# Performance work log

Hardware: AMD Instinct MI355X
Metric: run time of the kernel (lower is better)

Reference implementation:

```python
import jax, jax.numpy as jnp
import numpy as np

N, E, FS = 50000, 400000, 256
H, D = 8, 64            # GAT heads, hidden_size (per-head out_feats)
NH, DK, DV = 8, 64, 64  # transformer MHA
B = 1024
NEG_SLOPE = 0.2
EPS = 1e-6


def _layer_norm(x, g, b, eps=EPS):
    mu = x.mean(-1, keepdims=True)
    var = x.var(-1, keepdims=True)
    return (x - mu) / jnp.sqrt(var + eps) * g + b


def setup_inputs() -> dict:
    key = jax.random.key(0)
    ks = jax.random.split(key, 20)
    s = 0.02
    return {
        "features": jax.random.normal(ks[0], (N, FS), jnp.float32),
        "src": jax.random.randint(ks[1], (E,), 0, N, jnp.int32),
        "dst": jax.random.randint(ks[2], (E,), 0, N, jnp.int32),
        "url": jax.random.randint(ks[3], (B,), 1, N + 1, jnp.int32),  # 1-based ids
        # GATConv params (DGL-style)
        "gat_fc_w": jax.random.normal(ks[4], (FS, H * D), jnp.float32) * s,
        "attn_l": jax.random.normal(ks[5], (H, D), jnp.float32) * s,
        "attn_r": jax.random.normal(ks[6], (H, D), jnp.float32) * s,
        "gat_res_w": jax.random.normal(ks[7], (FS, H * D), jnp.float32) * s,
        "gat_bias": jnp.zeros((H, D), jnp.float32),
        # post-GAT LayerNorm
        "ln_g": jnp.ones((D,), jnp.float32),
        "ln_b": jnp.zeros((D,), jnp.float32),
        # MultiHeadAttention params
        "wq": jax.random.normal(ks[8], (D, NH * DK), jnp.float32) * s,
        "wk": jax.random.normal(ks[9], (D, NH * DK), jnp.float32) * s,
        "wv": jax.random.normal(ks[10], (D, NH * DV), jnp.float32) * s,
        "fc_w": jax.random.normal(ks[11], (NH * DV, D), jnp.float32) * s,
        "fc_b": jnp.zeros((D,), jnp.float32),
        "mha_ln_g": jnp.ones((D,), jnp.float32),
        "mha_ln_b": jnp.zeros((D,), jnp.float32),
        # final classifier
        "out_w": jax.random.normal(ks[12], (D, 2), jnp.float32) * s,
        "out_b": jnp.zeros((2,), jnp.float32),
    }


def reference(features, src, dst, url, gat_fc_w, attn_l, attn_r, gat_res_w,
              gat_bias, ln_g, ln_b, wq, wk, wv, fc_w, fc_b, mha_ln_g,
              mha_ln_b, out_w, out_b):
    # ---- GATConv (residual=True, bias, negative_slope=0.2, no activation) ----
    feat = (features @ gat_fc_w).reshape(N, H, D)          # [N,H,D]
    el = jnp.einsum('nhd,hd->nh', feat, attn_l)            # [N,H]
    er = jnp.einsum('nhd,hd->nh', feat, attn_r)            # [N,H]
    e = jax.nn.leaky_relu(el[src] + er[dst], NEG_SLOPE)    # [E,H] edge scores
    # segment softmax over incoming edges of each dst node
    m = jax.ops.segment_max(e, dst, num_segments=N)        # [N,H]
    m = jnp.where(jnp.isfinite(m), m, 0.0)
    ex = jnp.exp(e - m[dst])                               # [E,H]
    denom = jax.ops.segment_sum(ex, dst, num_segments=N)   # [N,H]
    a = ex / jnp.maximum(denom[dst], 1e-20)                # [E,H]
    msg = feat[src] * a[:, :, None]                        # [E,H,D]
    rst = jax.ops.segment_sum(msg, dst, num_segments=N)    # [N,H,D]
    res = (features @ gat_res_w).reshape(N, H, D)
    gat_emb = rst + res + gat_bias                         # [N,H,D]

    # ---- select batch nodes (url is 1-based) ----
    ids = url - 1
    x = gat_emb[ids]                                       # [B,H,D]
    x = _layer_norm(x, ln_g, ln_b)

    # ---- dense multi-head self-attention over the H gat heads (seq dim) ----
    residual = x
    q = (x @ wq).reshape(B, H, NH, DK)
    k = (x @ wk).reshape(B, H, NH, DK)
    v = (x @ wv).reshape(B, H, NH, DV)
    attn = jnp.einsum('bqhd,bkhd->bhqk', q, k) / jnp.sqrt(jnp.float32(DK))
    attn = jax.nn.softmax(attn, axis=-1)
    o = jnp.einsum('bhqk,bkhd->bqhd', attn, v).reshape(B, H, NH * DV)
    o = o @ fc_w + fc_b                                    # [B,H,D]
    o = _layer_norm(o + residual, mha_ln_g, mha_ln_b)

    # ---- pool + classify ----
    pooled = o.sum(axis=1)                                 # [B,D]
    logits = pooled @ out_w + out_b                        # [B,2]
    return logits
```

## Files before the change

kernel.cpp:

```cpp
#include <hip/hip_runtime.h>
#include <math.h>

#define Nn 50000
#define Ee 400000
#define FSz 256
#define HD_ 512
#define Bb 1024
#define HSZ 2048

static __device__ __forceinline__ int clampi(int v, int lo, int hi){
    return v < lo ? lo : (v > hi ? hi : v);
}
static __device__ __forceinline__ unsigned short f2bf(float f){
    unsigned int u = __float_as_uint(f);
    unsigned int r = u + 0x7FFFu + ((u >> 16) & 1u);
    return (unsigned short)(r >> 16);
}
static __device__ __forceinline__ float bflo(unsigned int v){ return __uint_as_float(v << 16); }
static __device__ __forceinline__ float bfhi(unsigned int v){ return __uint_as_float(v & 0xFFFF0000u); }

__global__ __launch_bounds__(256) void k_scatter(const int* __restrict__ src, const int* __restrict__ dst,
                                                 const int* __restrict__ url,
                                                 int* __restrict__ fill, int* __restrict__ slist,
                                                 const float* __restrict__ W,
                                                 const float* __restrict__ al,
                                                 const float* __restrict__ ar,
                                                 float* __restrict__ wl, float* __restrict__ wr,
                                                 const float* __restrict__ Wfc,
                                                 const float* __restrict__ Wres,
                                                 unsigned int* __restrict__ wfcb,
                                                 unsigned int* __restrict__ wresb){
    int t = threadIdx.x;
    if(blockIdx.x >= 1579){
        int bi = blockIdx.x - 1579;
        int m = bi >> 4;
        const float2* Sf = (const float2*)(m ? Wres : Wfc);
        unsigned int* D = m ? wresb : wfcb;
        int base = (bi & 15) * 8192;
        #pragma unroll
        for(int i = 0; i < 32; i++){
            int idx = base + i*256 + t;
            float2 v = Sf[idx];
            D[idx] = ((unsigned int)f2bf(v.y) << 16) | (unsigned int)f2bf(v.x);
        }
        return;
    }
    if(blockIdx.x >= 1563){
        int bi = blockIdx.x - 1563;
        int wv = t >> 6, lane = t & 63;
        #pragma unroll
        for(int r = 0; r < 4; r++){
            int f = bi*16 + wv*4 + r;
            float pl[8], pr[8];
            #pragma unroll
            for(int h = 0; h < 8; h++){
                float w = W[f*512 + h*64 + lane];
                pl[h] = w * al[h*64 + lane];
                pr[h] = w * ar[h*64 + lane];
            }
            #pragma unroll
            for(int h = 0; h < 8; h++){
                #pragma unroll
                for(int m = 32; m >= 1; m >>= 1){
                    pl[h] += __shfl_xor(pl[h], m, 64);
                    pr[h] += __shfl_xor(pr[h], m, 64);
                }
            }
            #pragma unroll
            for(int h = 0; h < 8; h++){
                if(lane == h){ wl[h*256 + f] = pl[h]; wr[h*256 + f] = pr[h]; }
            }
        }
        return;
    }
    __shared__ int key[HSZ];
    __shared__ int chainhead[HSZ];
    __shared__ short nxt[Bb];
    for(int i = t; i < HSZ; i += 256){ key[i] = -1; chainhead[i] = -1; }
    __syncthreads();
    for(int b = t; b < Bb; b += 256){
        int n = clampi(url[b] - 1, 0, Nn - 1);
        int h = n & (HSZ - 1);
        while(true){
            int prev = atomicCAS(&key[h], -1, n);
            if(prev == -1 || prev == n) break;
            h = (h + 1) & (HSZ - 1);
        }
        int old = atomicExch(&chainhead[h], b);
        nxt[b] = (short)old;
    }
    __syncthreads();
    int e = blockIdx.x * 256 + t;
    if(e >= Ee) return;
    int d = dst[e];
    if((unsigned)d >= (unsigned)Nn) return;
    int h = d & (HSZ - 1);
    while(true){
        int k = key[h];
        if(k == -1) return;
        if(k == d) break;
        h = (h + 1) & (HSZ - 1);
    }
    int s = clampi(src[e], 0, Nn - 1);
    for(int b = chainhead[h]; b != -1; b = nxt[b]){
        int pos = atomicAdd(&fill[b], 1);
        if(pos < 64) slist[b*64 + pos] = s;
    }
}

__global__ __launch_bounds__(256) void k_gat(const float* __restrict__ features,
                                             const unsigned int* __restrict__ Wfcb,
                                             const unsigned int* __restrict__ Wresb,
                                             const float* __restrict__ bias,
                                             const float* __restrict__ wl,
                                             const float* __restrict__ wr,
                                             const int* __restrict__ url,
                                             const int* __restrict__ fill, const int* __restrict__ slist,
                                             float* __restrict__ gemb){
    int t = threadIdx.x;
    int lane = t & 63, wv = t >> 6;
    int u0 = blockIdx.x * 2;

    __shared__ float cxs[2][8][256];
    __shared__ float fres[2][256];
    __shared__ float sew[2][64][8];
    __shared__ float ser[2][8];
    __shared__ int   sslist[2][64];

    for(int i = t; i < 2*64*8; i += 256) ((float*)sew)[i] = 0.f;

    float4 rwl[8], rwr[8];
    #pragma unroll
    for(int h = 0; h < 8; h++){
        rwl[h] = *(const float4*)&wl[h*256 + 4*lane];
        rwr[h] = *(const float4*)&wr[h*256 + 4*lane];
    }

    int dg[2], nj[2];
    #pragma unroll
    for(int j = 0; j < 2; j++){
        int u = u0 + j;
        dg[j] = min(fill[u], 64);
        nj[j] = clampi(url[u] - 1, 0, Nn - 1);
        if(t < dg[j]) sslist[j][t] = slist[u*64 + t];
        fres[j][t] = features[(size_t)nj[j] * FSz + t];
    }
    __syncthreads();

    int c1 = dg[0];
    int total = c1 + dg[1];
    for(int tau = wv; tau < total + 2; tau += 4){
        int j, i, isEr = 0;
        if(tau < c1){ j = 0; i = tau; }
        else if(tau < total){ j = 1; i = tau - c1; }
        else { j = tau - total; i = 0; isEr = 1; }
        int s = isEr ? nj[j] : sslist[j][i];
        float4 x = *(const float4*)(features + (size_t)s * FSz + 4*lane);
        float p[8];
        if(isEr){
            #pragma unroll
            for(int h = 0; h < 8; h++)
                p[h] = x.x*rwr[h].x + x.y*rwr[h].y + x.z*rwr[h].z + x.w*rwr[h].w;
        } else {
            #pragma unroll
            for(int h = 0; h < 8; h++)
                p[h] = x.x*rwl[h].x + x.y*rwl[h].y + x.z*rwl[h].z + x.w*rwl[h].w;
        }
        #pragma unroll
        for(int h = 0; h < 8; h++){
            #pragma unroll
            for(int m = 32; m >= 1; m >>= 1) p[h] += __shfl_xor(p[h], m, 64);
        }
        if(lane == 0){
            if(isEr){
                #pragma unroll
                for(int h = 0; h < 8; h++) ser[j][h] = p[h];
            } else {
                #pragma unroll
                for(int h = 0; h < 8; h++) sew[j][i][h] = p[h];
            }
        }
    }
    __syncthreads();
    if(t < 16){
        int j = t >> 3, h = t & 7;
        int dgj = dg[j];
        if(dgj > 0){
            float ern = ser[j][h];
            float m = -1e30f;
            for(int i = 0; i < dgj; i++){
                float v = sew[j][i][h] + ern;
                v = v > 0.f ? v : 0.2f * v;
                m = fmaxf(m, v);
            }
            float sum = 0.f;
            for(int i = 0; i < dgj; i++){
                float v = sew[j][i][h] + ern;
                v = v > 0.f ? v : 0.2f * v;
                float w = expf(v - m);
                sum += w;
                sew[j][i][h] = w;
            }
            float inv = 1.0f / fmaxf(sum, 1e-20f);
            for(int i = 0; i < dgj; i++) sew[j][i][h] *= inv;
        }
    }
    __syncthreads();
    {
        float cx[2][8];
        #pragma unroll
        for(int j = 0; j < 2; j++)
            #pragma unroll
            for(int h = 0; h < 8; h++) cx[j][h] = 0.f;
        int mxd = max(dg[0], dg[1]);
        for(int i = 0; i < mxd; i += 2){
            float x[2][2];
            #pragma unroll
            for(int j = 0; j < 2; j++)
                #pragma unroll
                for(int ii = 0; ii < 2; ii++){
                    int idx = i + ii;
                    int s = (idx < dg[j]) ? sslist[j][idx] : 0;
                    x[j][ii] = features[(size_t)s * FSz + t];
                }
            #pragma unroll
            for(int j = 0; j < 2; j++)
                #pragma unroll
                for(int ii = 0; ii < 2; ii++){
                    int idx = i + ii;
                    const float* av = &sew[j][idx < 64 ? idx : 0][0];
                    float xm = (idx < dg[j]) ? x[j][ii] : 0.f;
                    #pragma unroll
                    for(int h = 0; h < 8; h++) cx[j][h] += av[h] * xm;
                }
        }
        #pragma unroll
        for(int j = 0; j < 2; j++)
            #pragma unroll
            for(int h = 0; h < 8; h++) cxs[j][h][t] = cx[j][h];
    }
    __syncthreads();

    int h = t >> 5;
    int o0 = 2 * t;
    float a[2][2] = {{0,0},{0,0}};
    for(int f = 0; f < 256; f += 4){
        unsigned int w0 = Wfcb[(f+0)*256 + t];
        unsigned int w1 = Wfcb[(f+1)*256 + t];
        unsigned int w2 = Wfcb[(f+2)*256 + t];
        unsigned int w3 = Wfcb[(f+3)*256 + t];
        unsigned int r0 = Wresb[(f+0)*256 + t];
        unsigned int r1 = Wresb[(f+1)*256 + t];
        unsigned int r2 = Wresb[(f+2)*256 + t];
        unsigned int r3 = Wresb[(f+3)*256 + t];
        #pragma unroll
        for(int j = 0; j < 2; j++){
            float4 c = *(const float4*)&cxs[j][h][f];
            float4 x = *(const float4*)&fres[j][f];
            a[j][0] += c.x*bflo(w0) + c.y*bflo(w1) + c.z*bflo(w2) + c.w*bflo(w3)
                     + x.x*bflo(r0) + x.y*bflo(r1) + x.z*bflo(r2) + x.w*bflo(r3);
            a[j][1] += c.x*bfhi(w0) + c.y*bfhi(w1) + c.z*bfhi(w2) + c.w*bfhi(w3)
                     + x.x*bfhi(r0) + x.y*bfhi(r1) + x.z*bfhi(r2) + x.w*bfhi(r3);
        }
    }
    float b0 = bias[o0], b1 = bias[o0 + 1];
    #pragma unroll
    for(int j = 0; j < 2; j++){
        float2* gp = (float2*)(gemb + (size_t)(u0 + j) * HD_);
        gp[t] = make_float2(a[j][0] + b0, a[j][1] + b1);
    }
}

__global__ __launch_bounds__(256, 4) void k_mha(const float* __restrict__ gemb,
                                             const float* __restrict__ lng, const float* __restrict__ lnb,
                                             const float* __restrict__ wq, const float* __restrict__ wk,
                                             const float* __restrict__ wvp, const float* __restrict__ fcw,
                                             const float* __restrict__ fcb, const float* __restrict__ mlg,
                                             const float* __restrict__ mlb, const float* __restrict__ outw,
                                             const float* __restrict__ outb, float* __restrict__ out){
    __shared__ float A[512];
    __shared__ float xnF[512];
    __shared__ unsigned short xnT[512];
    __shared__ unsigned short qkb[8320];
    __shared__ float mu8[8], rs8[8], pooled[64];

    int t = threadIdx.x;
    int wv = t >> 6;
    int e = blockIdx.x;

    {
        const float* g0 = gemb + (size_t)e * HD_;
        A[t] = g0[t]; A[t + 256] = g0[t + 256];
    }
    __syncthreads();
    if(t < 64){
        int q = t >> 3, d0 = t & 7;
        float s = 0.f, s2 = 0.f;
        #pragma unroll
        for(int k = 0; k < 8; k++){ float v = A[q*64 + d0 + 8*k]; s += v; s2 += v * v; }
        #pragma unroll
        for(int m = 1; m <= 4; m <<= 1){ s += __shfl_xor(s, m, 64); s2 += __shfl_xor(s2, m, 64); }
        if(d0 == 0){
            float mu = s * (1.0f/64.0f);
            float var = s2 * (1.0f/64.0f) - mu * mu;
            mu8[q] = mu; rs8[q] = rsqrtf(fmaxf(var, 0.0f) + 1e-6f);
        }
    }
    __syncthreads();
    #pragma unroll
    for(int p = 0; p < 2; p++){
        int i = p*256 + t; int q = i >> 6, d = i & 63;
        float xv = (A[i] - mu8[q]) * rs8[q] * lng[d] + lnb[d];
        xnF[i] = xv;
        xnT[d*8 + q] = f2bf(xv);
    }
    __syncthreads();
    float aq0[8], aq1[8], ak0[8], ak1[8], av0[8], av1[8];
    #pragma unroll
    for(int r = 0; r < 8; r++){
        aq0[r]=0.f; aq1[r]=0.f; ak0[r]=0.f;
        ak1[r]=0.f; av0[r]=0.f; av1[r]=0.f;
    }
    #pragma unroll 2
    for(int d = 0; d < 64; d++){
        float q0 = wq[d*512 + t],  q1 = wq[d*512 + t + 256];
        float k0 = wk[d*512 + t],  k1 = wk[d*512 + t + 256];
        float v0 = wvp[d*512 + t], v1 = wvp[d*512 + t + 256];
        uint4 xp = *(const uint4*)&xnT[d*8];
        float xv[8] = { bflo(xp.x), bfhi(xp.x), bflo(xp.y), bfhi(xp.y),
                        bflo(xp.z), bfhi(xp.z), bflo(xp.w), bfhi(xp.w) };
        #pragma unroll
        for(int r = 0; r < 8; r++){
            aq0[r] += xv[r]*q0; aq1[r] += xv[r]*q1;
            ak0[r] += xv[r]*k0; ak1[r] += xv[r]*k1;
            av0[r] += xv[r]*v0; av1[r] += xv[r]*v1;
        }
    }
    #pragma unroll
    for(int qq = 0; qq < 8; qq++){
        qkb[qq*520 + t]              = f2bf(aq0[qq]);
        qkb[qq*520 + t + 256]        = f2bf(aq1[qq]);
        qkb[4160 + qq*520 + t]       = f2bf(ak0[qq]);
        qkb[4160 + qq*520 + t + 256] = f2bf(ak1[qq]);
    }
    __syncthreads();
    #pragma unroll
    for(int p = 0; p < 2; p++){
        int idx = p*256 + t;
        int nh = idx >> 6, qq = (idx >> 3) & 7, kk = idx & 7;
        const unsigned short* qrow = &qkb[qq*520 + nh*64];
        const unsigned short* krow = &qkb[4160 + kk*520 + nh*64];
        float s = 0.f;
        #pragma unroll
        for(int d8 = 0; d8 < 64; d8 += 8){
            uint4 qv = *(const uint4*)&qrow[d8];
            uint4 kv = *(const uint4*)&krow[d8];
            s += bflo(qv.x)*bflo(kv.x) + bfhi(qv.x)*bfhi(kv.x)
               + bflo(qv.y)*bflo(kv.y) + bfhi(qv.y)*bfhi(kv.y)
               + bflo(qv.z)*bflo(kv.z) + bfhi(qv.z)*bfhi(kv.z)
               + bflo(qv.w)*bflo(kv.w) + bfhi(qv.w)*bfhi(kv.w);
        }
        A[idx] = s * 0.125f;
    }
    __syncthreads();
    if(t < 64){
        int row = t;
        float mx = -1e30f;
        #pragma unroll
        for(int k = 0; k < 8; k++) mx = fmaxf(mx, A[row*8 + k]);
        float ev[8]; float s = 0.f;
        #pragma unroll
        for(int k = 0; k < 8; k++){ ev[k] = expf(A[row*8 + k] - mx); s += ev[k]; }
        float inv = 1.0f / s;
        #pragma unroll
        for(int k = 0; k < 8; k++) A[row*8 + k] = ev[k] * inv;
    }
    __syncthreads();
    {
        int nh0 = wv;
        #pragma unroll
        for(int qq = 0; qq < 8; qq++){
            const float* s0 = &A[nh0*64 + qq*8];
            const float* s1 = &A[(nh0+4)*64 + qq*8];
            float4 a0 = *(const float4*)s0, b0 = *(const float4*)(s0 + 4);
            float4 a1 = *(const float4*)s1, b1 = *(const float4*)(s1 + 4);
            float o0 = a0.x*av0[0] + a0.y*av0[1] + a0.z*av0[2] + a0.w*av0[3]
                     + b0.x*av0[4] + b0.y*av0[5] + b0.z*av0[6] + b0.w*av0[7];
            float o1 = a1.x*av1[0] + a1.y*av1[1] + a1.z*av1[2] + a1.w*av1[3]
                     + b1.x*av1[4] + b1.y*av1[5] + b1.z*av1[6] + b1.w*av1[7];
            qkb[qq*520 + t]       = f2bf(o0);
            qkb[qq*520 + t + 256] = f2bf(o1);
        }
    }
    __syncthreads();
    {
        float* P = (float*)&qkb[4160];
        int g = (t & 63) & 31;
        int qh = (t & 63) >> 5;
        int k0r = wv * 128;
        float a[4][2];
        #pragma unroll
        for(int jq = 0; jq < 4; jq++){ a[jq][0] = 0.f; a[jq][1] = 0.f; }
        const float2* fw2 = (const float2*)fcw;
        for(int k = k0r; k < k0r + 128; k += 8){
            float2 f0 = fw2[(k+0)*32 + g];
            float2 f1 = fw2[(k+1)*32 + g];
            float2 f2 = fw2[(k+2)*32 + g];
            float2 f3 = fw2[(k+3)*32 + g];
            float2 f4 = fw2[(k+4)*32 + g];
            float2 f5 = fw2[(k+5)*32 + g];
            float2 f6 = fw2[(k+6)*32 + g];
            float2 f7 = fw2[(k+7)*32 + g];
            #pragma unroll
            for(int jq = 0; jq < 4; jq++){
                int qq = qh*4 + jq;
                uint4 op = *(const uint4*)&qkb[qq*520 + k];
                float x0 = bflo(op.x), x1 = bfhi(op.x), x2 = bflo(op.y), x3 = bfhi(op.y);
                float x4 = bflo(op.z), x5 = bfhi(op.z), x6 = bflo(op.w), x7 = bfhi(op.w);
                a[jq][0] += x0*f0.x + x1*f1.x + x2*f2.x + x3*f3.x + x4*f4.x + x5*f5.x + x6*f6.x + x7*f7.x;
                a[jq][1] += x0*f0.y + x1*f1.y + x2*f2.y + x3*f3.y + x4*f4.y + x5*f5.y + x6*f6.y + x7*f7.y;
            }
        }
        __syncthreads();
        #pragma unroll
        for(int jq = 0; jq < 4; jq++){
            int qq = qh*4 + jq;
            *(float2*)&P[wv*512 + qq*64 + 2*g] = make_float2(a[jq][0], a[jq][1]);
        }
        __syncthreads();
        #pragma unroll
        for(int p = 0; p < 2; p++){
            int o = p*256 + t; int dd = o & 63;
            A[o] = P[o] + P[512 + o] + P[1024 + o] + P[1536 + o] + fcb[dd] + xnF[o];
        }
    }
    __syncthreads();
    if(t < 64){
        int q = t >> 3, d0 = t & 7;
        float s = 0.f, s2 = 0.f;
        #pragma unroll
        for(int k = 0; k < 8; k++){ float v = A[q*64 + d0 + 8*k]; s += v; s2 += v * v; }
        #pragma unroll
        for(int m = 1; m <= 4; m <<= 1){ s += __shfl_xor(s, m, 64); s2 += __shfl_xor(s2, m, 64); }
        if(d0 == 0){
            float mu = s * (1.0f/64.0f);
            float var = s2 * (1.0f/64.0f) - mu * mu;
            mu8[q] = mu; rs8[q] = rsqrtf(fmaxf(var, 0.0f) + 1e-6f);
        }
    }
    __syncthreads();
    if(t < 64){
        int dd = t;
        float g2 = mlg[dd], bb = mlb[dd];
        float s = 0.f;
        #pragma unroll
        for(int qq = 0; qq < 8; qq++)
            s += (A[qq*64 + dd] - mu8[qq]) * rs8[qq] * g2 + bb;
        pooled[dd] = s;
    }
    __syncthreads();
    if(t < 128){
        int c = t >> 6, d = t & 63;
        float v = pooled[d] * outw[d*2 + c];
        #pragma unroll
        for(int m = 32; m >= 1; m >>= 1) v += __shfl_xor(v, m, 64);
        if((t & 63) == 0) out[e*2 + c] = v + outb[c];
    }
}

extern "C" void kernel_launch(void* const* d_in, const int* in_sizes, int n_in,
                              void* d_out, int out_size, void* d_ws, size_t ws_size,
                              hipStream_t stream){
    (void)in_sizes; (void)n_in; (void)out_size; (void)ws_size;
    const float* features  = (const float*)d_in[0];
    const int*   src       = (const int*)d_in[1];
    const int*   dst       = (const int*)d_in[2];
    const int*   url       = (const int*)d_in[3];
    const float* gat_fc_w  = (const float*)d_in[4];
    const float* attn_l    = (const float*)d_in[5];
    const float* attn_r    = (const float*)d_in[6];
    const float* gat_res_w = (const float*)d_in[7];
    const float* gat_bias  = (const float*)d_in[8];
    const float* ln_g      = (const float*)d_in[9];
    const float* ln_b      = (const float*)d_in[10];
    const float* wq        = (const float*)d_in[11];
    const float* wk        = (const float*)d_in[12];
    const float* wv        = (const float*)d_in[13];
    const float* fc_w      = (const float*)d_in[14];
    const float* fc_b      = (const float*)d_in[15];
    const float* mha_ln_g  = (const float*)d_in[16];
    const float* mha_ln_b  = (const float*)d_in[17];
    const float* out_w     = (const float*)d_in[18];
    const float* out_b     = (const float*)d_in[19];

    char* base = (char*)d_ws;
    size_t cur = 0;
    auto alloc = [&](size_t nbytes) -> void* {
        void* p = base + cur;
        cur = (cur + nbytes + 255) & ~(size_t)255;
        return p;
    };
    float*        wl    = (float*)alloc(2048 * sizeof(float));
    float*        wr    = (float*)alloc(2048 * sizeof(float));
    int*          fill  = (int*)alloc(1024 * sizeof(int));
    int*          slist = (int*)alloc((size_t)1024 * 64 * sizeof(int));
    float*        gemb  = (float*)alloc((size_t)1024 * 512 * sizeof(float));
    unsigned int* wfcb  = (unsigned int*)alloc((size_t)256 * 512 * sizeof(unsigned short));
    unsigned int* wresb = (unsigned int*)alloc((size_t)256 * 512 * sizeof(unsigned short));

    hipMemsetAsync(fill, 0, 1024 * sizeof(int), stream);

    hipLaunchKernelGGL(k_scatter, dim3(1611), dim3(256), 0, stream, src, dst, url, fill, slist,
                       gat_fc_w, attn_l, attn_r, wl, wr, gat_fc_w, gat_res_w, wfcb, wresb);
    hipLaunchKernelGGL(k_gat,     dim3(512),  dim3(256), 0, stream, features, wfcb, wresb, gat_bias,
                       wl, wr, url, fill, slist, gemb);
    hipLaunchKernelGGL(k_mha,     dim3(1024), dim3(256), 0, stream, gemb, ln_g, ln_b,
                       wq, wk, wv, fc_w, fc_b, mha_ln_g, mha_ln_b, out_w, out_b,
                       (float*)d_out);
}
```

Baseline: 208.0 us.

## Process one batch node per GAT block and parallelize edge softmax across lanes

The GAT kernel now handles one batch node per block instead of two, doubling the grid to 1024 blocks and adding a launch bound of 4 blocks per SM. The per-head edge softmax moves from 16 serial threads to 64 threads that split edges and combine results with shuffle reductions. The aggregation loop is unrolled by 4 gathers instead of 2 per node. These changes aim to raise parallelism and occupancy and cut the serial softmax latency. In exchange, the bf16 weight matrices are streamed once per node instead of once per pair of nodes, doubling weight traffic.

```diff
diff --git a/kernel.cpp b/kernel.cpp
--- a/kernel.cpp
+++ b/kernel.cpp
@@ -108,7 +108,7 @@
     }
 }
 
-__global__ __launch_bounds__(256) void k_gat(const float* __restrict__ features,
+__global__ __launch_bounds__(256, 4) void k_gat(const float* __restrict__ features,
                                              const unsigned int* __restrict__ Wfcb,
                                              const unsigned int* __restrict__ Wresb,
                                              const float* __restrict__ bias,
@@ -119,15 +119,15 @@
                                              float* __restrict__ gemb){
     int t = threadIdx.x;
     int lane = t & 63, wv = t >> 6;
-    int u0 = blockIdx.x * 2;
-
-    __shared__ float cxs[2][8][256];
-    __shared__ float fres[2][256];
-    __shared__ float sew[2][64][8];
-    __shared__ float ser[2][8];
-    __shared__ int   sslist[2][64];
-
-    for(int i = t; i < 2*64*8; i += 256) ((float*)sew)[i] = 0.f;
+    int u = blockIdx.x;
+
+    __shared__ float cxs[8][256];
+    __shared__ float fres[256];
+    __shared__ float sew[64][8];
+    __shared__ float ser[8];
+    __shared__ int   sslist[64];
+
+    for(int i = t; i < 64*8; i += 256) ((float*)sew)[i] = 0.f;
 
     float4 rwl[8], rwr[8];
     #pragma unroll
@@ -136,25 +136,15 @@
         rwr[h] = *(const float4*)&wr[h*256 + 4*lane];
     }
 
-    int dg[2], nj[2];
-    #pragma unroll
-    for(int j = 0; j < 2; j++){
-        int u = u0 + j;
-        dg[j] = min(fill[u], 64);
-        nj[j] = clampi(url[u] - 1, 0, Nn - 1);
-        if(t < dg[j]) sslist[j][t] = slist[u*64 + t];
-        fres[j][t] = features[(size_t)nj[j] * FSz + t];
-    }
-    __syncthreads();
-
-    int c1 = dg[0];
-    int total = c1 + dg[1];
-    for(int tau = wv; tau < total + 2; tau += 4){
-        int j, i, isEr = 0;
-        if(tau < c1){ j = 0; i = tau; }
-        else if(tau < total){ j = 1; i = tau - c1; }
-        else { j = tau - total; i = 0; isEr = 1; }
-        int s = isEr ? nj[j] : sslist[j][i];
+    int dg = min(fill[u], 64);
+    int nj = clampi(url[u] - 1, 0, Nn - 1);
+    if(t < dg) sslist[t] = slist[u*64 + t];
+    fres[t] = features[(size_t)nj * FSz + t];
+    __syncthreads();
+
+    for(int tau = wv; tau < dg + 1; tau += 4){
+        int isEr = (tau == dg);
+        int s = isEr ? nj : sslist[tau];
         float4 x = *(const float4*)(features + (size_t)s * FSz + 4*lane);
         float p[8];
         if(isEr){
@@ -174,76 +164,67 @@
         if(lane == 0){
             if(isEr){
                 #pragma unroll
-                for(int h = 0; h < 8; h++) ser[j][h] = p[h];
+                for(int h = 0; h < 8; h++) ser[h] = p[h];
             } else {
                 #pragma unroll
-                for(int h = 0; h < 8; h++) sew[j][i][h] = p[h];
-            }
-        }
-    }
-    __syncthreads();
-    if(t < 16){
-        int j = t >> 3, h = t & 7;
-        int dgj = dg[j];
-        if(dgj > 0){
-            float ern = ser[j][h];
-            float m = -1e30f;
-            for(int i = 0; i < dgj; i++){
-                float v = sew[j][i][h] + ern;
-                v = v > 0.f ? v : 0.2f * v;
-                m = fmaxf(m, v);
-            }
-            float sum = 0.f;
-            for(int i = 0; i < dgj; i++){
-                float v = sew[j][i][h] + ern;
-                v = v > 0.f ? v : 0.2f * v;
-                float w = expf(v - m);
-                sum += w;
-                sew[j][i][h] = w;
-            }
-            float inv = 1.0f / fmaxf(sum, 1e-20f);
-            for(int i = 0; i < dgj; i++) sew[j][i][h] *= inv;
-        }
+                for(int h = 0; h < 8; h++) sew[tau][h] = p[h];
+            }
+        }
+    }
+    __syncthreads();
+    if(t < 64){
+        int h = t >> 3, il = t & 7;
+        float ern = ser[h];
+        float m = -1e30f;
+        for(int i = il; i < dg; i += 8){
+            float v = sew[i][h] + ern;
+            v = v > 0.f ? v : 0.2f * v;
+            m = fmaxf(m, v);
+        }
+        #pragma unroll
+        for(int mm = 1; mm <= 4; mm <<= 1) m = fmaxf(m, __shfl_xor(m, mm, 64));
+        float sum = 0.f;
+        for(int i = il; i < dg; i += 8){
+            float v = sew[i][h] + ern;
+            v = v > 0.f ? v : 0.2f * v;
+            float w = expf(v - m);
+            sum += w;
+            sew[i][h] = w;
+        }
+        #pragma unroll
+        for(int mm = 1; mm <= 4; mm <<= 1) sum += __shfl_xor(sum, mm, 64);
+        float inv = 1.0f / fmaxf(sum, 1e-20f);
+        for(int i = il; i < dg; i += 8) sew[i][h] *= inv;
     }
     __syncthreads();
     {
-        float cx[2][8];
-        #pragma unroll
-        for(int j = 0; j < 2; j++)
-            #pragma unroll
-            for(int h = 0; h < 8; h++) cx[j][h] = 0.f;
-        int mxd = max(dg[0], dg[1]);
-        for(int i = 0; i < mxd; i += 2){
-            float x[2][2];
-            #pragma unroll
-            for(int j = 0; j < 2; j++)
+        float cx[8];
+        #pragma unroll
+        for(int h = 0; h < 8; h++) cx[h] = 0.f;
+        for(int i = 0; i < dg; i += 4){
+            float x[4];
+            #pragma unroll
+            for(int ii = 0; ii < 4; ii++){
+                int idx = i + ii;
+                int s = (idx < dg) ? sslist[idx] : 0;
+                x[ii] = features[(size_t)s * FSz + t];
+            }
+            #pragma unroll
+            for(int ii = 0; ii < 4; ii++){
+                int idx = i + ii;
+                const float* av = &sew[idx < 64 ? idx : 0][0];
+                float xm = (idx < dg) ? x[ii] : 0.f;
                 #pragma unroll
-                for(int ii = 0; ii < 2; ii++){
-                    int idx = i + ii;
-                    int s = (idx < dg[j]) ? sslist[j][idx] : 0;
-                    x[j][ii] = features[(size_t)s * FSz + t];
-                }
-            #pragma unroll
-            for(int j = 0; j < 2; j++)
-                #pragma unroll
-                for(int ii = 0; ii < 2; ii++){
-                    int idx = i + ii;
-                    const float* av = &sew[j][idx < 64 ? idx : 0][0];
-                    float xm = (idx < dg[j]) ? x[j][ii] : 0.f;
-                    #pragma unroll
-                    for(int h = 0; h < 8; h++) cx[j][h] += av[h] * xm;
-                }
-        }
-        #pragma unroll
-        for(int j = 0; j < 2; j++)
-            #pragma unroll
-            for(int h = 0; h < 8; h++) cxs[j][h][t] = cx[j][h];
-    }
-    __syncthreads();
-
-    int h = t >> 5;
-    int o0 = 2 * t;
-    float a[2][2] = {{0,0},{0,0}};
+                for(int h = 0; h < 8; h++) cx[h] += av[h] * xm;
+            }
+        }
+        #pragma unroll
+        for(int h = 0; h < 8; h++) cxs[h][t] = cx[h];
+    }
+    __syncthreads();
+
+    int hh = t >> 5;
+    float a0 = 0.f, a1 = 0.f;
     for(int f = 0; f < 256; f += 4){
         unsigned int w0 = Wfcb[(f+0)*256 + t];
         unsigned int w1 = Wfcb[(f+1)*256 + t];
@@ -253,22 +234,15 @@
         unsigned int r1 = Wresb[(f+1)*256 + t];
         unsigned int r2 = Wresb[(f+2)*256 + t];
         unsigned int r3 = Wresb[(f+3)*256 + t];
-        #pragma unroll
-        for(int j = 0; j < 2; j++){
-            float4 c = *(const float4*)&cxs[j][h][f];
-            float4 x = *(const float4*)&fres[j][f];
-            a[j][0] += c.x*bflo(w0) + c.y*bflo(w1) + c.z*bflo(w2) + c.w*bflo(w3)
-                     + x.x*bflo(r0) + x.y*bflo(r1) + x.z*bflo(r2) + x.w*bflo(r3);
-            a[j][1] += c.x*bfhi(w0) + c.y*bfhi(w1) + c.z*bfhi(w2) + c.w*bfhi(w3)
-                     + x.x*bfhi(r0) + x.y*bfhi(r1) + x.z*bfhi(r2) + x.w*bfhi(r3);
-        }
-    }
-    float b0 = bias[o0], b1 = bias[o0 + 1];
-    #pragma unroll
-    for(int j = 0; j < 2; j++){
-        float2* gp = (float2*)(gemb + (size_t)(u0 + j) * HD_);
-        gp[t] = make_float2(a[j][0] + b0, a[j][1] + b1);
-    }
+        float4 c = *(const float4*)&cxs[hh][f];
+        float4 x = *(const float4*)&fres[f];
+        a0 += c.x*bflo(w0) + c.y*bflo(w1) + c.z*bflo(w2) + c.w*bflo(w3)
+            + x.x*bflo(r0) + x.y*bflo(r1) + x.z*bflo(r2) + x.w*bflo(r3);
+        a1 += c.x*bfhi(w0) + c.y*bfhi(w1) + c.z*bfhi(w2) + c.w*bfhi(w3)
+            + x.x*bfhi(r0) + x.y*bfhi(r1) + x.z*bfhi(r2) + x.w*bfhi(r3);
+    }
+    float2* gp = (float2*)(gemb + (size_t)u * HD_);
+    gp[t] = make_float2(a0 + bias[2*t], a1 + bias[2*t + 1]);
 }
 
 __global__ __launch_bounds__(256, 4) void k_mha(const float* __restrict__ gemb,
@@ -512,7 +486,7 @@
 
     hipLaunchKernelGGL(k_scatter, dim3(1611), dim3(256), 0, stream, src, dst, url, fill, slist,
                        gat_fc_w, attn_l, attn_r, wl, wr, gat_fc_w, gat_res_w, wfcb, wresb);
-    hipLaunchKernelGGL(k_gat,     dim3(512),  dim3(256), 0, stream, features, wfcb, wresb, gat_bias,
+    hipLaunchKernelGGL(k_gat,     dim3(1024), dim3(256), 0, stream, features, wfcb, wresb, gat_bias,
                        wl, wr, url, fill, slist, gemb);
     hipLaunchKernelGGL(k_mha,     dim3(1024), dim3(256), 0, stream, gemb, ln_g, ln_b,
                        wq, wk, wv, fc_w, fc_b, mha_ln_g, mha_ln_b, out_w, out_b,
```

Result: faster. 202.1 us (-2.8%).
